# Optimization experiments

Hardware: AMD Instinct MI355X
Metric: run time of the kernel (lower is better)

## Reference

```python
import jax, jax.numpy as jnp
import numpy as np

TARGET_SIZE = (240, 320)
SCALE = 8
POS_MARGIN = 1.0
NEG_MARGIN = 0.2
POS_LAMBDA = 0.05
EPS = 1e-12


def _l2n(x, axis):
    # F.normalize(p=2): x / max(||x||, eps)
    n = jnp.sqrt(jnp.sum(x * x, axis=axis, keepdims=True))
    return x / jnp.maximum(n, EPS)


def _rodrigues(rv):
    # axis-angle [N,3] -> rotation matrix [N,3,3]
    theta = jnp.linalg.norm(rv, axis=-1, keepdims=True)
    k = rv / jnp.maximum(theta, EPS)
    kx, ky, kz = k[..., 0], k[..., 1], k[..., 2]
    z = jnp.zeros_like(kx)
    Km = jnp.stack([z, -kz, ky, kz, z, -kx, -ky, kx, z], axis=-1).reshape(rv.shape[:-1] + (3, 3))
    th = theta[..., None]
    I = jnp.eye(3, dtype=rv.dtype)
    return I + jnp.sin(th) * Km + (1.0 - jnp.cos(th)) * (Km @ Km)


def _plane_homography(rv0, t0, rv1, t1, n, d, K, Kinv):
    # plane-induced homography: H = K (R_0->1 - t_0->1 n^T / d) K^{-1}
    R0 = _rodrigues(rv0)
    R1 = _rodrigues(rv1)
    R = R1 @ jnp.swapaxes(R0, -1, -2)
    t = t1[..., None] - R @ t0[..., None]            # [N,3,1]
    return K @ (R - (t @ n) / d[..., None]) @ Kinv   # n:[N,1,3], d:[N,1]


def _scale_homography(H, origin, target):
    # sizes are (H, W); homography acts on (x, y, 1): H' = S H S^{-1}
    s = target / origin                               # [N,2] = (sy, sx)
    svec = jnp.stack([s[:, 1], s[:, 0], jnp.ones_like(s[:, 0])], axis=-1)  # (sx, sy, 1)
    return H * (svec[:, :, None] / svec[:, None, :])


def _coord_cells(Hc, Wc):
    xx, yy = jnp.meshgrid(jnp.arange(Wc), jnp.arange(Hc), indexing='xy')
    return jnp.stack([xx, yy], axis=-1).astype(jnp.float32) * SCALE  # [Hc,Wc,2] (x,y)


def _forward(pred_features, rotation_vector, translation_vectors, camera_nts,
             camera_depths, camera_Ks, camera_Kinvs, origin_sizes, interval_list):
    T, B, C = rotation_vector.shape[:3]
    TC = T * C
    Cf, Hc, Wc = pred_features.shape[-3:]
    M = Hc * Wc

    # permute [T,B,C,...] -> [T,C,B,...] -> flatten to [T*C,B,...] (matches torch permute+reshape)
    rv = jnp.transpose(rotation_vector, (0, 2, 1, 3)).reshape(TC, B, 3)
    tv = jnp.transpose(translation_vectors, (0, 2, 1, 3)).reshape(TC, B, 3)
    nts = jnp.transpose(camera_nts, (0, 2, 1, 3, 4)).reshape(TC, B, 1, 3)
    dep = jnp.transpose(camera_depths, (0, 2, 1, 3)).reshape(TC, B, 1)
    Ks = jnp.transpose(camera_Ks, (0, 2, 1, 3, 4)).reshape(TC, B, 3, 3)
    Kin = jnp.transpose(camera_Kinvs, (0, 2, 1, 3, 4)).reshape(TC, B, 3, 3)
    osz = jnp.transpose(origin_sizes, (0, 2, 1, 3)).reshape(TC, B, 2)

    coords = _coord_cells(Hc, Wc)                     # [Hc,Wc,2]
    target = jnp.asarray(TARGET_SIZE, jnp.float32)
    thresh = SCALE - 0.5

    def step(acc, xs):
        f0, f1, Htt = xs                              # f0,f1: [B,Cf,Hc,Wc], Htt: [B,3,3]
        d0 = _l2n(f0, 1)
        d1 = _l2n(f1, 1)
        dot = jax.nn.relu(jnp.einsum('bchw,bcHW->bhwHW', d0, d1))  # [B,Hc,Wc,Hc,Wc]
        dot = _l2n(dot.reshape(B, Hc, Wc, M), 3).reshape(B, Hc, Wc, Hc, Wc)
        dot = _l2n(dot.reshape(B, M, Hc, Wc), 1).reshape(B, Hc, Wc, Hc, Wc)
        pos = jax.nn.relu(POS_MARGIN - dot)
        neg = jax.nn.relu(dot - NEG_MARGIN)
        # warp frame-0 cell centers into frame 1
        pts = jnp.concatenate([jnp.broadcast_to(coords, (B, Hc, Wc, 2)),
                               jnp.ones((B, Hc, Wc, 1), f0.dtype)], axis=-1)
        w = jnp.einsum('bij,bhwj->bhwi', Htt, pts)
        z = w[..., 2:3]
        z = jnp.where(jnp.abs(z) < 1e-8, 1e-8, z)
        warped = w[..., :2] / z                       # [B,Hc,Wc,2]
        dist = jnp.linalg.norm(coords[None, None, None] - warped[:, :, :, None, None, :], axis=-1)
        mask = (dist <= thresh).astype(dot.dtype)     # [B,Hc,Wc,Hc,Wc]
        l = POS_LAMBDA * mask * pos + (1.0 - mask) * neg
        return acc + jnp.mean(l), None

    total = jnp.float32(0.0)
    for interval in interval_list:
        iv = int(interval)
        N = TC - iv
        flat = lambda a: a[:N].reshape((N * B,) + a.shape[2:])
        H_all = _plane_homography(flat(rv), flat(tv),
                                  rv[iv:].reshape(N * B, 3), tv[iv:].reshape(N * B, 3),
                                  flat(nts), flat(dep), flat(Ks), flat(Kin))
        H_all = _scale_homography(H_all, flat(osz), jnp.broadcast_to(target, (N * B, 2)))
        loss_i, _ = jax.lax.scan(step, jnp.float32(0.0),
                                 (pred_features[:N], pred_features[iv:], H_all.reshape(N, B, 3, 3)))
        total = total + loss_i / N
    return total / len(interval_list)


def setup_inputs() -> dict:
    key = jax.random.key(0)
    ks = jax.random.split(key, 8)
    T, B, C, Cf = 5, 2, 4, 32
    Hc, Wc = TARGET_SIZE[0] // SCALE, TARGET_SIZE[1] // SCALE
    pred = jax.random.normal(ks[0], (T * C, B, Cf, Hc, Wc), jnp.float32)
    rv = 0.1 * jax.random.normal(ks[1], (T, B, C, 3), jnp.float32)
    tv = 0.1 * jax.random.normal(ks[2], (T, B, C, 3), jnp.float32)
    nts = jnp.array([0.0, 0.0, -1.0], jnp.float32) + 0.05 * jax.random.normal(ks[3], (T, B, C, 1, 3), jnp.float32)
    dep = 1.0 + jax.random.uniform(ks[4], (T, B, C, 1), jnp.float32)
    fx = 300.0 + 200.0 * jax.random.uniform(ks[5], (T, B, C), jnp.float32)
    fy = fx * (0.95 + 0.1 * jax.random.uniform(ks[6], (T, B, C), jnp.float32))
    K = jnp.zeros((T, B, C, 3, 3), jnp.float32)
    K = K.at[..., 0, 0].set(fx).at[..., 1, 1].set(fy)
    K = K.at[..., 0, 2].set(320.0).at[..., 1, 2].set(240.0).at[..., 2, 2].set(1.0)
    Kinv = jnp.linalg.inv(K)
    osz = jnp.tile(jnp.array([480.0, 640.0], jnp.float32), (T, B, C, 1))
    return {
        'pred_features': pred,
        'rotation_vector': rv,
        'translation_vectors': tv,
        'camera_nts': nts,
        'camera_depths': dep,
        'camera_Ks': K,
        'camera_Kinvs': Kinv,
        'origin_sizes': osz,
        'interval_list': (1, 4),
    }


def reference(pred_features, rotation_vector, translation_vectors, camera_nts,
              camera_depths, camera_Ks, camera_Kinvs, origin_sizes, interval_list):
    return _forward(pred_features, rotation_vector, translation_vectors, camera_nts,
                    camera_depths, camera_Ks, camera_Kinvs, origin_sizes, interval_list)
```

## Files before the change

kernel.cpp:

```cpp
#include <hip/hip_runtime.h>
#include <math.h>

#define TT   5
#define CAM  4
#define TC   20
#define BB   2
#define CF   32
#define HC   30
#define WC   40
#define MM   1200
#define NMAX 19
#define EPSF 1e-12f
#define JT   75
#define RG4  19
#define RGB4 5
#define JSP  5
#define JQ   15
#define CT   5
#define REDB 16

typedef __attribute__((ext_vector_type(8))) short short8v;
typedef __attribute__((ext_vector_type(4))) float float4v;

__device__ inline unsigned short f2bf(float x) {
  unsigned int u = __float_as_uint(x);
  unsigned int r = (u + 0x7FFFu + ((u >> 16) & 1u)) >> 16;
  return (unsigned short)r;
}
__device__ inline float bf2f(unsigned short h) {
  return __uint_as_float(((unsigned int)h) << 16);
}

__device__ inline void rodrigues_d(const double rv[3], double R[9]) {
  double th = sqrt(rv[0]*rv[0] + rv[1]*rv[1] + rv[2]*rv[2]);
  double thc = fmax(th, 1e-12);
  double kx = rv[0] / thc, ky = rv[1] / thc, kz = rv[2] / thc;
  double st = sin(th), ct = cos(th);
  double Km[9] = { 0.0, -kz,  ky,  kz, 0.0, -kx,  -ky, kx, 0.0 };
  double K2[9];
  for (int r = 0; r < 3; ++r)
    for (int c = 0; c < 3; ++c)
      K2[r*3+c] = Km[r*3+0]*Km[0*3+c] + Km[r*3+1]*Km[1*3+c] + Km[r*3+2]*Km[2*3+c];
  for (int r = 0; r < 3; ++r)
    for (int c = 0; c < 3; ++c)
      R[r*3+c] = (r == c ? 1.0 : 0.0) + st * Km[r*3+c] + (1.0 - ct) * K2[r*3+c];
}
__device__ inline void mm3(const double* A, const double* B, double* C) {
  for (int r = 0; r < 3; ++r)
    for (int c = 0; c < 3; ++c)
      C[r*3+c] = A[r*3+0]*B[0*3+c] + A[r*3+1]*B[1*3+c] + A[r*3+2]*B[2*3+c];
}

__device__ inline bool decode_slot(int slot, const int* ivl, int& n, int& b, int& iv) {
  int ivi = slot / (NMAX * BB);
  int rem = slot % (NMAX * BB);
  n = rem / BB; b = rem % BB;
  iv = ivl[ivi];
  return n < TC - iv;
}

__global__ void k_prep(const float* __restrict__ pred, short8v* __restrict__ dsp,
                       const float* __restrict__ rv_, const float* __restrict__ tv_,
                       const float* __restrict__ nts_, const float* __restrict__ dep_,
                       const float* __restrict__ Ks_, const float* __restrict__ Kin_,
                       const float* __restrict__ osz_, const int* __restrict__ ivl,
                       float2* __restrict__ warped) {
  int bx = blockIdx.x;
  int tid = threadIdx.x;
  if (bx < TC * BB * 5) {
    int tb = bx / 5;
    int pix = (bx % 5) * 240 + tid;
    if (tid >= 240 || pix >= MM) return;
    const float* src = pred + (size_t)tb * CF * MM;
    short8v*     dst = dsp  + (size_t)tb * 4 * MM;
    float v[CF]; float ss = 0.f;
#pragma unroll
    for (int c = 0; c < CF; ++c) { float x = src[c * MM + pix]; v[c] = x; ss = fmaf(x, x, ss); }
    float inv = 1.f / fmaxf(sqrtf(ss), EPSF);
#pragma unroll
    for (int s = 0; s < 4; ++s) {
      short8v oh;
#pragma unroll
      for (int e = 0; e < 8; ++e) oh[e] = (short)f2bf(v[s*8+e] * inv);
      dst[(size_t)s * MM + pix] = oh;
    }
    return;
  }
  int slot = bx - TC * BB * 5;
  int n, b, iv;
  if (!decode_slot(slot, ivl, n, b, iv)) return;
  int q0 = n, q1 = n + iv;
  int t0 = q0 / CAM, c0 = q0 % CAM;
  int t1 = q1 / CAM, c1 = q1 % CAM;
  size_t e0 = (size_t)(t0 * BB + b) * CAM + c0;
  size_t e1 = (size_t)(t1 * BB + b) * CAM + c1;

  double rv0[3], tv0[3], rv1[3], tv1[3], nv[3];
  for (int k = 0; k < 3; ++k) {
    rv0[k] = rv_[e0*3 + k]; tv0[k] = tv_[e0*3 + k];
    rv1[k] = rv_[e1*3 + k]; tv1[k] = tv_[e1*3 + k];
    nv[k]  = nts_[e0*3 + k];
  }
  double d = dep_[e0];
  double K9[9], Ki9[9];
  for (int k = 0; k < 9; ++k) { K9[k] = Ks_[e0*9 + k]; Ki9[k] = Kin_[e0*9 + k]; }

  double R0[9], R1[9], R[9];
  rodrigues_d(rv0, R0);
  rodrigues_d(rv1, R1);
  for (int r = 0; r < 3; ++r)
    for (int c = 0; c < 3; ++c)
      R[r*3+c] = R1[r*3+0]*R0[c*3+0] + R1[r*3+1]*R0[c*3+1] + R1[r*3+2]*R0[c*3+2];
  double tvec[3];
  for (int r = 0; r < 3; ++r)
    tvec[r] = tv1[r] - (R[r*3+0]*tv0[0] + R[r*3+1]*tv0[1] + R[r*3+2]*tv0[2]);
  double Mid[9];
  for (int r = 0; r < 3; ++r)
    for (int c = 0; c < 3; ++c)
      Mid[r*3+c] = R[r*3+c] - tvec[r] * nv[c] / d;
  double T1[9], Hm[9];
  mm3(K9, Mid, T1);
  mm3(T1, Ki9, Hm);

  double osz0 = osz_[e0*2 + 0], osz1 = osz_[e0*2 + 1];
  double s0 = 240.0 / osz0, s1 = 320.0 / osz1;
  double sv[3] = { s1, s0, 1.0 };
  double Hs[9];
  for (int r = 0; r < 3; ++r)
    for (int c = 0; c < 3; ++c)
      Hs[r*3+c] = Hm[r*3+c] * sv[r] / sv[c];

  float2* wout = warped + (size_t)slot * MM;
  for (int cell = tid; cell < MM; cell += blockDim.x) {
    double x = (double)((cell % WC) * 8);
    double y = (double)((cell / WC) * 8);
    double wx = Hs[0]*x + Hs[1]*y + Hs[2];
    double wy = Hs[3]*x + Hs[4]*y + Hs[5];
    double wz = Hs[6]*x + Hs[7]*y + Hs[8];
    float z = (float)wz;
    if (fabsf(z) < 1e-8f) z = 1e-8f;
    wout[cell] = make_float2((float)wx / z, (float)wy / z);
  }
}

__device__ inline float4v s_tile1(short8v ah, short8v bh) {
  float4v acc = {0.f, 0.f, 0.f, 0.f};
  return __builtin_amdgcn_mfma_f32_16x16x32_bf16(ah, bh, acc, 0, 0, 0);
}

__global__ void __launch_bounds__(256) k_rnorm_p(const short8v* __restrict__ dsp,
                                                 const int* __restrict__ ivl,
                                                 float* __restrict__ prn) {
  int slot = blockIdx.x, jh = blockIdx.z;
  int n, b, iv;
  if (!decode_slot(slot, ivl, n, b, iv)) return;
  int wid = threadIdx.x >> 6, lane = threadIdx.x & 63;
  int rg = blockIdx.y * 4 + wid;
  if (rg >= RG4) return;
  int q = lane >> 4, li = lane & 15;
  int base = rg * 64;
  const short8v* D0 = dsp + (size_t)(n * BB + b) * 4 * MM;
  const short8v* B0 = dsp + (size_t)((n + iv) * BB + b) * 4 * MM + (size_t)q * MM + li;
  bool vt[4]; int rt[4];
  short8v ah[4];
  float4v racc[4];
#pragma unroll
  for (int t = 0; t < 4; ++t) {
    int rb = base + t * 16;
    vt[t] = rb < MM;
    rt[t] = vt[t] ? rb : 0;
    ah[t] = D0[(size_t)q * MM + rt[t] + li];
    racc[t] = (float4v){0.f, 0.f, 0.f, 0.f};
  }
  int jt0 = jh * JQ, jtN = jt0 + JQ;
  short8v bA = B0[jt0 * 16];
  short8v bB = B0[min(jt0 + 1, JT - 1) * 16];
#pragma unroll 3
  for (int jt = jt0; jt < jtN; ++jt) {
    short8v bC = B0[min(jt + 2, JT - 1) * 16];
#pragma unroll
    for (int t = 0; t < 4; ++t) {
      float4v acc = s_tile1(ah[t], bA);
#pragma unroll
      for (int r = 0; r < 4; ++r) {
        float x = fmaxf(acc[r], 0.f);
        racc[t][r] = fmaf(x, x, racc[t][r]);
      }
    }
    bA = bB; bB = bC;
  }
#pragma unroll
  for (int m = 1; m <= 8; m <<= 1)
#pragma unroll
    for (int t = 0; t < 4; ++t)
#pragma unroll
      for (int r = 0; r < 4; ++r)
        racc[t][r] += __shfl_xor(racc[t][r], m);
  if (li == 0) {
    float* o = prn + ((size_t)slot * JSP + jh) * MM;
#pragma unroll
    for (int t = 0; t < 4; ++t)
      if (vt[t]) {
#pragma unroll
        for (int r = 0; r < 4; ++r) o[rt[t] + q * 4 + r] = racc[t][r];
      }
  }
}

__global__ void __launch_bounds__(256) k_rnorm_fin(const float* __restrict__ prn,
                                                   const int* __restrict__ ivl,
                                                   float* __restrict__ irn) {
  int slot = blockIdx.x;
  int n, b, iv;
  if (!decode_slot(slot, ivl, n, b, iv)) return;
  int row = blockIdx.y * 256 + threadIdx.x;
  if (row >= MM) return;
  const float* p = prn + (size_t)slot * JSP * MM;
  float s = 0.f;
#pragma unroll
  for (int k = 0; k < JSP; ++k) s += p[k * MM + row];
  irn[(size_t)slot * MM + row] = 1.f / fmaxf(sqrtf(s), EPSF);
}

__global__ void __launch_bounds__(256) k_cnorm_p(const short8v* __restrict__ dsp,
                                                 const int* __restrict__ ivl,
                                                 const float* __restrict__ irn,
                                                 float* __restrict__ pcn) {
  int slot = blockIdx.x, jh = blockIdx.z;
  int n, b, iv;
  if (!decode_slot(slot, ivl, n, b, iv)) return;
  int wid = threadIdx.x >> 6, lane = threadIdx.x & 63;
  int rg = blockIdx.y * 4 + wid;
  if (rg >= RG4) return;
  int q = lane >> 4, li = lane & 15;
  int base = rg * 64;
  const short8v* D1 = dsp + (size_t)((n + iv) * BB + b) * 4 * MM;
  const short8v* B0 = dsp + (size_t)(n * BB + b) * 4 * MM + (size_t)q * MM + li;
  bool vt[4]; int rt[4];
  short8v ah[4];
  float4v cacc[4];
#pragma unroll
  for (int t = 0; t < 4; ++t) {
    int rb = base + t * 16;
    vt[t] = rb < MM;
    rt[t] = vt[t] ? rb : 0;
    ah[t] = D1[(size_t)q * MM + rt[t] + li];
    cacc[t] = (float4v){0.f, 0.f, 0.f, 0.f};
  }
  const float* irnS = irn + (size_t)slot * MM + li;
  int jt0 = jh * JQ, jtN = jt0 + JQ;
  short8v bA = B0[jt0 * 16];
  short8v bB = B0[min(jt0 + 1, JT - 1) * 16];
  float irA = irnS[jt0 * 16];
  float irB = irnS[min(jt0 + 1, JT - 1) * 16];
#pragma unroll 3
  for (int jt = jt0; jt < jtN; ++jt) {
    short8v bC = B0[min(jt + 2, JT - 1) * 16];
    float irC = irnS[min(jt + 2, JT - 1) * 16];
#pragma unroll
    for (int t = 0; t < 4; ++t) {
      float4v acc = s_tile1(ah[t], bA);
#pragma unroll
      for (int r = 0; r < 4; ++r) {
        float x = fmaxf(acc[r], 0.f) * irA;
        cacc[t][r] = fmaf(x, x, cacc[t][r]);
      }
    }
    bA = bB; bB = bC; irA = irB; irB = irC;
  }
#pragma unroll
  for (int m = 1; m <= 8; m <<= 1)
#pragma unroll
    for (int t = 0; t < 4; ++t)
#pragma unroll
      for (int r = 0; r < 4; ++r)
        cacc[t][r] += __shfl_xor(cacc[t][r], m);
  if (li == 0) {
    float* o = pcn + ((size_t)slot * JSP + jh) * MM;
#pragma unroll
    for (int t = 0; t < 4; ++t)
      if (vt[t]) {
#pragma unroll
        for (int r = 0; r < 4; ++r) o[rt[t] + q * 4 + r] = cacc[t][r];
      }
  }
}

__global__ void __launch_bounds__(256) k_cnorm_fin(const float* __restrict__ pcn,
                                                   const int* __restrict__ ivl,
                                                   float* __restrict__ icn) {
  int slot = blockIdx.x;
  int n, b, iv;
  if (!decode_slot(slot, ivl, n, b, iv)) return;
  int col = blockIdx.y * 256 + threadIdx.x;
  if (col >= MM) return;
  const float* p = pcn + (size_t)slot * JSP * MM;
  float s = 0.f;
#pragma unroll
  for (int k = 0; k < JSP; ++k) s += p[k * MM + col];
  icn[(size_t)slot * MM + col] = 1.f / fmaxf(sqrtf(s), EPSF);
}

__global__ void __launch_bounds__(256) k_loss(const short8v* __restrict__ dsp,
                                              const int* __restrict__ ivl,
                                              const float* __restrict__ irn,
                                              const float* __restrict__ icn,
                                              int niv,
                                              double* __restrict__ partials) {
  int slot = blockIdx.x, jh = blockIdx.z;
  int wid = threadIdx.x >> 6, lane = threadIdx.x & 63;
  int rg = blockIdx.y * 4 + wid;
  if (rg >= RG4) return;
  size_t pidx = ((size_t)slot * RG4 + rg) * JSP + jh;
  int n, b, iv;
  if (!decode_slot(slot, ivl, n, b, iv)) {
    if (lane == 0) partials[pidx] = 0.0;
    return;
  }
  int q = lane >> 4, li = lane & 15;
  int base = rg * 64;
  const short8v* D0 = dsp + (size_t)(n * BB + b) * 4 * MM;
  const short8v* B0 = dsp + (size_t)((n + iv) * BB + b) * 4 * MM + (size_t)q * MM + li;
  short8v ah[4];
  float u[4][4];
#pragma unroll
  for (int t = 0; t < 4; ++t) {
    int rb = base + t * 16;
    bool vt = rb < MM;
    int rtc = vt ? rb : 0;
    ah[t] = D0[(size_t)q * MM + rtc + li];
#pragma unroll
    for (int r = 0; r < 4; ++r)
      u[t][r] = vt ? irn[(size_t)slot * MM + rtc + q * 4 + r] : 0.f;
  }
  const float* icnS = icn + (size_t)slot * MM + li;
  int jt0 = jh * JQ, jtN = jt0 + JQ;
  short8v bA = B0[jt0 * 16];
  short8v bB = B0[min(jt0 + 1, JT - 1) * 16];
  float icA = icnS[jt0 * 16];
  float icB = icnS[min(jt0 + 1, JT - 1) * 16];
  float lacc0 = 0.f, lacc1 = 0.f;
#pragma unroll 3
  for (int jt = jt0; jt < jtN; ++jt) {
    short8v bC = B0[min(jt + 2, JT - 1) * 16];
    float icC = icnS[min(jt + 2, JT - 1) * 16];
#pragma unroll
    for (int t = 0; t < 4; ++t) {
      float4v acc = s_tile1(ah[t], bA);
      float s0 = fmaxf(fmaf(acc[0], icA * u[t][0], -0.2f), 0.f)
               + fmaxf(fmaf(acc[1], icA * u[t][1], -0.2f), 0.f);
      float s1 = fmaxf(fmaf(acc[2], icA * u[t][2], -0.2f), 0.f)
               + fmaxf(fmaf(acc[3], icA * u[t][3], -0.2f), 0.f);
      lacc0 += s0; lacc1 += s1;
    }
    bA = bB; bB = bC; icA = icB; icB = icC;
  }
  float lacc = lacc0 + lacc1;
#pragma unroll
  for (int off = 32; off > 0; off >>= 1) lacc += __shfl_xor(lacc, off);
  if (lane == 0) {
    double scale = 1.0 / ((double)(TC - iv) * BB * (double)MM * (double)MM * (double)niv);
    partials[pidx] = (double)lacc * scale;
  }
}

__global__ void __launch_bounds__(256) k_corr(const short8v* __restrict__ dsp,
                                              const int* __restrict__ ivl,
                                              const float* __restrict__ irn,
                                              const float* __restrict__ icn,
                                              const float2* __restrict__ warped,
                                              int niv,
                                              double* __restrict__ partials2) {
  __shared__ double swsum[4];
  int slot = blockIdx.x, tile = blockIdx.y;
  int t = threadIdx.x;
  int n, b, iv;
  bool valid = decode_slot(slot, ivl, n, b, iv);
  double corr = 0.0;
  int row = tile * 256 + t;
  if (valid && row < MM) {
    float2 wp = warped[(size_t)slot * MM + row];
    int kx0 = max(0, (int)ceilf((wp.x - 7.5f) * 0.125f));
    int kx1 = min(WC - 1, (int)floorf((wp.x + 7.5f) * 0.125f));
    int ky0 = max(0, (int)ceilf((wp.y - 7.5f) * 0.125f));
    int ky1 = min(HC - 1, (int)floorf((wp.y + 7.5f) * 0.125f));
    if (kx0 <= kx1 && ky0 <= ky1) {
      const short8v* D0 = dsp + (size_t)(n * BB + b) * 4 * MM;
      const short8v* D1 = dsp + (size_t)((n + iv) * BB + b) * 4 * MM;
      float a[CF];
#pragma unroll
      for (int qq = 0; qq < 4; ++qq) {
        short8v h = D0[(size_t)qq * MM + row];
#pragma unroll
        for (int e = 0; e < 8; ++e) a[qq * 8 + e] = bf2f((unsigned short)h[e]);
      }
      float ir = irn[(size_t)slot * MM + row];
      float fcorr = 0.f;
      for (int ky = ky0; ky <= ky1; ++ky) {
        for (int kx = kx0; kx <= kx1; ++kx) {
          float dx = (float)(kx * 8) - wp.x;
          float dy = (float)(ky * 8) - wp.y;
          if (fmaf(dx, dx, dy * dy) <= 56.25f) {
            int j = ky * WC + kx;
            float dot = 0.f;
#pragma unroll
            for (int qq = 0; qq < 4; ++qq) {
              short8v h1 = D1[(size_t)qq * MM + j];
#pragma unroll
              for (int e = 0; e < 8; ++e)
                dot = fmaf(a[qq * 8 + e], bf2f((unsigned short)h1[e]), dot);
            }
            float s = fmaxf(dot, 0.f);
            float D = s * ir * icn[(size_t)slot * MM + j];
            fcorr += 0.05f * fmaxf(1.f - D, 0.f) - fmaxf(D - 0.2f, 0.f);
          }
        }
      }
      double scale = 1.0 / ((double)(TC - iv) * BB * (double)MM * (double)MM * (double)niv);
      corr = (double)fcorr * scale;
    }
  }
#pragma unroll
  for (int off = 32; off > 0; off >>= 1) corr += __shfl_down(corr, off);
  int wid = t >> 6, lane = t & 63;
  if (lane == 0) swsum[wid] = corr;
  __syncthreads();
  if (t == 0) partials2[(size_t)slot * CT + tile] = swsum[0] + swsum[1] + swsum[2] + swsum[3];
}

__global__ void __launch_bounds__(256) k_red1(const double* __restrict__ p1, int n1,
                                              const double* __restrict__ p2, int n2,
                                              double* __restrict__ red) {
  __shared__ double sw[4];
  int t = threadIdx.x, blk = blockIdx.x;
  double s = 0.0;
  for (int i = blk * 256 + t; i < n1; i += REDB * 256) s += p1[i];
  for (int i = blk * 256 + t; i < n2; i += REDB * 256) s += p2[i];
#pragma unroll
  for (int off = 32; off > 0; off >>= 1) s += __shfl_down(s, off);
  int wid = t >> 6, lane = t & 63;
  if (lane == 0) sw[wid] = s;
  __syncthreads();
  if (t == 0) red[blk] = sw[0] + sw[1] + sw[2] + sw[3];
}

__global__ void k_red2(const double* __restrict__ red, float* __restrict__ out) {
  int lane = threadIdx.x;
  double s = (lane < REDB) ? red[lane] : 0.0;
#pragma unroll
  for (int off = 32; off > 0; off >>= 1) s += __shfl_down(s, off);
  if (lane == 0) out[0] = (float)s;
}

extern "C" void kernel_launch(void* const* d_in, const int* in_sizes, int n_in,
                              void* d_out, int out_size, void* d_ws, size_t ws_size,
                              hipStream_t stream) {
  const float* pred = (const float*)d_in[0];
  const float* rv   = (const float*)d_in[1];
  const float* tv   = (const float*)d_in[2];
  const float* nts  = (const float*)d_in[3];
  const float* dep  = (const float*)d_in[4];
  const float* Ks   = (const float*)d_in[5];
  const float* Kin  = (const float*)d_in[6];
  const float* osz  = (const float*)d_in[7];
  const int*   ivl  = (const int*)d_in[8];
  int niv = in_sizes[8];
  int slots = niv * NMAX * BB;

  char* ws = (char*)d_ws;
  size_t off = 0;
  short8v* dsp = (short8v*)(ws + off);  off += (size_t)TC * BB * 4 * MM * 16;
  float2* warped = (float2*)(ws + off); off += (size_t)slots * MM * 8;
  float* prn = (float*)(ws + off);      off += (size_t)slots * JSP * MM * 4;
  float* pcn = (float*)(ws + off);      off += (size_t)slots * JSP * MM * 4;
  float* irn = (float*)(ws + off);      off += (size_t)slots * MM * 4;
  float* icn = (float*)(ws + off);      off += (size_t)slots * MM * 4;
  off = (off + 255) & ~(size_t)255;
  double* partials = (double*)(ws + off);  off += (size_t)slots * RG4 * JSP * 8;
  double* partials2 = (double*)(ws + off); off += (size_t)slots * CT * 8;
  double* red = (double*)(ws + off);       off += (size_t)REDB * 8;

  int n1 = slots * RG4 * JSP;
  int n2 = slots * CT;

  hipLaunchKernelGGL(k_prep, dim3(TC * BB * 5 + slots), dim3(256), 0, stream,
                     pred, dsp, rv, tv, nts, dep, Ks, Kin, osz, ivl, warped);
  dim3 sgrid(slots, RGB4, JSP);
  dim3 fgrid(slots, CT);
  hipLaunchKernelGGL(k_rnorm_p, sgrid, dim3(256), 0, stream, dsp, ivl, prn);
  hipLaunchKernelGGL(k_rnorm_fin, fgrid, dim3(256), 0, stream, prn, ivl, irn);
  hipLaunchKernelGGL(k_cnorm_p, sgrid, dim3(256), 0, stream, dsp, ivl, irn, pcn);
  hipLaunchKernelGGL(k_cnorm_fin, fgrid, dim3(256), 0, stream, pcn, ivl, icn);
  hipLaunchKernelGGL(k_loss, sgrid, dim3(256), 0, stream, dsp, ivl, irn, icn, niv, partials);
  hipLaunchKernelGGL(k_corr, fgrid, dim3(256), 0, stream,
                     dsp, ivl, irn, icn, warped, niv, partials2);
  hipLaunchKernelGGL(k_red1, dim3(REDB), dim3(256), 0, stream, partials, n1, partials2, n2, red);
  hipLaunchKernelGGL(k_red2, dim3(1), dim3(64), 0, stream, red, (float*)d_out);
}
```

Measured before the change: 76.90 us.

## Fuse norm finalisation into consumers and merge loss, correlation and reductions

The separate row and column inverse-norm finalise kernels are removed. Each consumer now sums the split partial norms itself, into shared memory or registers, using rsqrt. The loss and correlation kernels are merged into a single launch that uses an extra grid z-slice, and the row scale is pre-multiplied into the bf16 A fragments. The two-stage final reduction becomes one block. Together these cut the launch count from nine to five, at the cost of redundant partial-sum reads and an extra bf16 rounding of the scaled features, which may change numerics slightly.

Measured after the change: 75.52 us. No clear change (-1.8%).

```diff
diff --git a/kernel.cpp b/kernel.cpp
--- a/kernel.cpp
+++ b/kernel.cpp
@@ -11,13 +11,13 @@
 #define MM   1200
 #define NMAX 19
 #define EPSF 1e-12f
+#define EPS2 1e-24f
 #define JT   75
 #define RG4  19
 #define RGB4 5
 #define JSP  5
 #define JQ   15
 #define CT   5
-#define REDB 16
 
 typedef __attribute__((ext_vector_type(8))) short short8v;
 typedef __attribute__((ext_vector_type(4))) float float4v;
@@ -174,10 +174,10 @@
   }
   int jt0 = jh * JQ, jtN = jt0 + JQ;
   short8v bA = B0[jt0 * 16];
-  short8v bB = B0[min(jt0 + 1, JT - 1) * 16];
+  short8v bB = B0[min(jt0 + 1, jtN - 1) * 16];
 #pragma unroll 3
   for (int jt = jt0; jt < jtN; ++jt) {
-    short8v bC = B0[min(jt + 2, JT - 1) * 16];
+    short8v bC = B0[min(jt + 2, jtN - 1) * 16];
 #pragma unroll
     for (int t = 0; t < 4; ++t) {
       float4v acc = s_tile1(ah[t], bA);
@@ -207,29 +207,26 @@
   }
 }
 
-__global__ void __launch_bounds__(256) k_rnorm_fin(const float* __restrict__ prn,
-                                                   const int* __restrict__ ivl,
-                                                   float* __restrict__ irn) {
-  int slot = blockIdx.x;
-  int n, b, iv;
-  if (!decode_slot(slot, ivl, n, b, iv)) return;
-  int row = blockIdx.y * 256 + threadIdx.x;
-  if (row >= MM) return;
-  const float* p = prn + (size_t)slot * JSP * MM;
-  float s = 0.f;
-#pragma unroll
-  for (int k = 0; k < JSP; ++k) s += p[k * MM + row];
-  irn[(size_t)slot * MM + row] = 1.f / fmaxf(sqrtf(s), EPSF);
-}
-
 __global__ void __launch_bounds__(256) k_cnorm_p(const short8v* __restrict__ dsp,
                                                  const int* __restrict__ ivl,
-                                                 const float* __restrict__ irn,
+                                                 const float* __restrict__ prn,
                                                  float* __restrict__ pcn) {
+  __shared__ float sIR[240];
   int slot = blockIdx.x, jh = blockIdx.z;
   int n, b, iv;
   if (!decode_slot(slot, ivl, n, b, iv)) return;
-  int wid = threadIdx.x >> 6, lane = threadIdx.x & 63;
+  int t = threadIdx.x;
+  int jt0 = jh * JQ, jtN = jt0 + JQ;
+  const float* prnS = prn + (size_t)slot * JSP * MM;
+  if (t < 240) {
+    int i = jt0 * 16 + t;
+    float s = 0.f;
+#pragma unroll
+    for (int k = 0; k < JSP; ++k) s += prnS[k * MM + i];
+    sIR[t] = rsqrtf(fmaxf(s, EPS2));
+  }
+  __syncthreads();
+  int wid = t >> 6, lane = t & 63;
   int rg = blockIdx.y * 4 + wid;
   if (rg >= RG4) return;
   int q = lane >> 4, li = lane & 15;
@@ -240,30 +237,29 @@
   short8v ah[4];
   float4v cacc[4];
 #pragma unroll
-  for (int t = 0; t < 4; ++t) {
-    int rb = base + t * 16;
-    vt[t] = rb < MM;
-    rt[t] = vt[t] ? rb : 0;
-    ah[t] = D1[(size_t)q * MM + rt[t] + li];
-    cacc[t] = (float4v){0.f, 0.f, 0.f, 0.f};
-  }
-  const float* irnS = irn + (size_t)slot * MM + li;
-  int jt0 = jh * JQ, jtN = jt0 + JQ;
+  for (int tt = 0; tt < 4; ++tt) {
+    int rb = base + tt * 16;
+    vt[tt] = rb < MM;
+    rt[tt] = vt[tt] ? rb : 0;
+    ah[tt] = D1[(size_t)q * MM + rt[tt] + li];
+    cacc[tt] = (float4v){0.f, 0.f, 0.f, 0.f};
+  }
   short8v bA = B0[jt0 * 16];
-  short8v bB = B0[min(jt0 + 1, JT - 1) * 16];
-  float irA = irnS[jt0 * 16];
-  float irB = irnS[min(jt0 + 1, JT - 1) * 16];
+  short8v bB = B0[min(jt0 + 1, jtN - 1) * 16];
+  float irA = sIR[li];
+  float irB = sIR[(min(jt0 + 1, jtN - 1) - jt0) * 16 + li];
 #pragma unroll 3
   for (int jt = jt0; jt < jtN; ++jt) {
-    short8v bC = B0[min(jt + 2, JT - 1) * 16];
-    float irC = irnS[min(jt + 2, JT - 1) * 16];
-#pragma unroll
-    for (int t = 0; t < 4; ++t) {
-      float4v acc = s_tile1(ah[t], bA);
+    int jn = min(jt + 2, jtN - 1);
+    short8v bC = B0[jn * 16];
+    float irC = sIR[(jn - jt0) * 16 + li];
+#pragma unroll
+    for (int tt = 0; tt < 4; ++tt) {
+      float4v acc = s_tile1(ah[tt], bA);
 #pragma unroll
       for (int r = 0; r < 4; ++r) {
         float x = fmaxf(acc[r], 0.f) * irA;
-        cacc[t][r] = fmaf(x, x, cacc[t][r]);
+        cacc[tt][r] = fmaf(x, x, cacc[tt][r]);
       }
     }
     bA = bB; bB = bC; irA = irB; irB = irC;
@@ -271,87 +267,161 @@
 #pragma unroll
   for (int m = 1; m <= 8; m <<= 1)
 #pragma unroll
-    for (int t = 0; t < 4; ++t)
+    for (int tt = 0; tt < 4; ++tt)
 #pragma unroll
       for (int r = 0; r < 4; ++r)
-        cacc[t][r] += __shfl_xor(cacc[t][r], m);
+        cacc[tt][r] += __shfl_xor(cacc[tt][r], m);
   if (li == 0) {
     float* o = pcn + ((size_t)slot * JSP + jh) * MM;
 #pragma unroll
-    for (int t = 0; t < 4; ++t)
-      if (vt[t]) {
-#pragma unroll
-        for (int r = 0; r < 4; ++r) o[rt[t] + q * 4 + r] = cacc[t][r];
+    for (int tt = 0; tt < 4; ++tt)
+      if (vt[tt]) {
+#pragma unroll
+        for (int r = 0; r < 4; ++r) o[rt[tt] + q * 4 + r] = cacc[tt][r];
       }
   }
 }
 
-__global__ void __launch_bounds__(256) k_cnorm_fin(const float* __restrict__ pcn,
-                                                   const int* __restrict__ ivl,
-                                                   float* __restrict__ icn) {
-  int slot = blockIdx.x;
+__global__ void __launch_bounds__(256) k_lc(const short8v* __restrict__ dsp,
+                                            const int* __restrict__ ivl,
+                                            const float* __restrict__ prn,
+                                            const float* __restrict__ pcn,
+                                            const float2* __restrict__ warped,
+                                            int niv,
+                                            double* __restrict__ partials,
+                                            double* __restrict__ partials2) {
+  __shared__ float sIC[240];
+  __shared__ float sLIR[256];
+  __shared__ double swsum[4];
+  int slot = blockIdx.x, y = blockIdx.y, z = blockIdx.z;
+  int t = threadIdx.x;
   int n, b, iv;
-  if (!decode_slot(slot, ivl, n, b, iv)) return;
-  int col = blockIdx.y * 256 + threadIdx.x;
-  if (col >= MM) return;
-  const float* p = pcn + (size_t)slot * JSP * MM;
-  float s = 0.f;
-#pragma unroll
-  for (int k = 0; k < JSP; ++k) s += p[k * MM + col];
-  icn[(size_t)slot * MM + col] = 1.f / fmaxf(sqrtf(s), EPSF);
-}
-
-__global__ void __launch_bounds__(256) k_loss(const short8v* __restrict__ dsp,
-                                              const int* __restrict__ ivl,
-                                              const float* __restrict__ irn,
-                                              const float* __restrict__ icn,
-                                              int niv,
-                                              double* __restrict__ partials) {
-  int slot = blockIdx.x, jh = blockIdx.z;
-  int wid = threadIdx.x >> 6, lane = threadIdx.x & 63;
-  int rg = blockIdx.y * 4 + wid;
+  bool valid = decode_slot(slot, ivl, n, b, iv);
+  const float* prnS = prn + (size_t)slot * JSP * MM;
+  const float* pcnS = pcn + (size_t)slot * JSP * MM;
+
+  if (z == JSP) {
+    double corr = 0.0;
+    int row = y * 256 + t;
+    if (valid && row < MM) {
+      float2 wp = warped[(size_t)slot * MM + row];
+      int kx0 = max(0, (int)ceilf((wp.x - 7.5f) * 0.125f));
+      int kx1 = min(WC - 1, (int)floorf((wp.x + 7.5f) * 0.125f));
+      int ky0 = max(0, (int)ceilf((wp.y - 7.5f) * 0.125f));
+      int ky1 = min(HC - 1, (int)floorf((wp.y + 7.5f) * 0.125f));
+      if (kx0 <= kx1 && ky0 <= ky1) {
+        const short8v* D0 = dsp + (size_t)(n * BB + b) * 4 * MM;
+        const short8v* D1 = dsp + (size_t)((n + iv) * BB + b) * 4 * MM;
+        float a[CF];
+#pragma unroll
+        for (int qq = 0; qq < 4; ++qq) {
+          short8v h = D0[(size_t)qq * MM + row];
+#pragma unroll
+          for (int e = 0; e < 8; ++e) a[qq * 8 + e] = bf2f((unsigned short)h[e]);
+        }
+        float irs = 0.f;
+#pragma unroll
+        for (int k = 0; k < JSP; ++k) irs += prnS[k * MM + row];
+        float ir = rsqrtf(fmaxf(irs, EPS2));
+        float fcorr = 0.f;
+        for (int ky = ky0; ky <= ky1; ++ky) {
+          for (int kx = kx0; kx <= kx1; ++kx) {
+            float dx = (float)(kx * 8) - wp.x;
+            float dy = (float)(ky * 8) - wp.y;
+            if (fmaf(dx, dx, dy * dy) <= 56.25f) {
+              int j = ky * WC + kx;
+              float dot = 0.f;
+#pragma unroll
+              for (int qq = 0; qq < 4; ++qq) {
+                short8v h1 = D1[(size_t)qq * MM + j];
+#pragma unroll
+                for (int e = 0; e < 8; ++e)
+                  dot = fmaf(a[qq * 8 + e], bf2f((unsigned short)h1[e]), dot);
+              }
+              float ics = 0.f;
+#pragma unroll
+              for (int k = 0; k < JSP; ++k) ics += pcnS[k * MM + j];
+              float ic = rsqrtf(fmaxf(ics, EPS2));
+              float s = fmaxf(dot, 0.f);
+              float D = s * ir * ic;
+              fcorr += 0.05f * fmaxf(1.f - D, 0.f) - fmaxf(D - 0.2f, 0.f);
+            }
+          }
+        }
+        double scale = 1.0 / ((double)(TC - iv) * BB * (double)MM * (double)MM * (double)niv);
+        corr = (double)fcorr * scale;
+      }
+    }
+#pragma unroll
+    for (int off = 32; off > 0; off >>= 1) corr += __shfl_down(corr, off);
+    int wid = t >> 6, lane = t & 63;
+    if (lane == 0) swsum[wid] = corr;
+    __syncthreads();
+    if (t == 0) partials2[(size_t)slot * CT + y] = swsum[0] + swsum[1] + swsum[2] + swsum[3];
+    return;
+  }
+
+  int wid = t >> 6, lane = t & 63;
+  int rg = y * 4 + wid;
+  if (!valid) {
+    if (lane == 0 && rg < RG4) partials[((size_t)slot * RG4 + rg) * JSP + z] = 0.0;
+    return;
+  }
+  int jt0 = z * JQ, jtN = jt0 + JQ;
+  if (t < 240) {
+    int j = jt0 * 16 + t;
+    float s = 0.f;
+#pragma unroll
+    for (int k = 0; k < JSP; ++k) s += pcnS[k * MM + j];
+    sIC[t] = rsqrtf(fmaxf(s, EPS2));
+  }
+  {
+    int row = y * 256 + t;
+    float v = 0.f;
+    if (row < MM) {
+      float s = 0.f;
+#pragma unroll
+      for (int k = 0; k < JSP; ++k) s += prnS[k * MM + row];
+      v = rsqrtf(fmaxf(s, EPS2));
+    }
+    sLIR[t] = v;
+  }
+  __syncthreads();
   if (rg >= RG4) return;
-  size_t pidx = ((size_t)slot * RG4 + rg) * JSP + jh;
-  int n, b, iv;
-  if (!decode_slot(slot, ivl, n, b, iv)) {
-    if (lane == 0) partials[pidx] = 0.0;
-    return;
-  }
   int q = lane >> 4, li = lane & 15;
   int base = rg * 64;
   const short8v* D0 = dsp + (size_t)(n * BB + b) * 4 * MM;
   const short8v* B0 = dsp + (size_t)((n + iv) * BB + b) * 4 * MM + (size_t)q * MM + li;
   short8v ah[4];
-  float u[4][4];
-#pragma unroll
-  for (int t = 0; t < 4; ++t) {
-    int rb = base + t * 16;
+#pragma unroll
+  for (int t4 = 0; t4 < 4; ++t4) {
+    int rb = base + t4 * 16;
     bool vt = rb < MM;
     int rtc = vt ? rb : 0;
-    ah[t] = D0[(size_t)q * MM + rtc + li];
-#pragma unroll
-    for (int r = 0; r < 4; ++r)
-      u[t][r] = vt ? irn[(size_t)slot * MM + rtc + q * 4 + r] : 0.f;
-  }
-  const float* icnS = icn + (size_t)slot * MM + li;
-  int jt0 = jh * JQ, jtN = jt0 + JQ;
+    short8v a = D0[(size_t)q * MM + rtc + li];
+    float sc = vt ? sLIR[wid * 64 + t4 * 16 + li] : 0.f;
+#pragma unroll
+    for (int e = 0; e < 8; ++e)
+      a[e] = (short)f2bf(bf2f((unsigned short)a[e]) * sc);
+    ah[t4] = a;
+  }
   short8v bA = B0[jt0 * 16];
-  short8v bB = B0[min(jt0 + 1, JT - 1) * 16];
-  float icA = icnS[jt0 * 16];
-  float icB = icnS[min(jt0 + 1, JT - 1) * 16];
+  short8v bB = B0[min(jt0 + 1, jtN - 1) * 16];
+  float icA = sIC[li];
+  float icB = sIC[(min(jt0 + 1, jtN - 1) - jt0) * 16 + li];
   float lacc0 = 0.f, lacc1 = 0.f;
 #pragma unroll 3
   for (int jt = jt0; jt < jtN; ++jt) {
-    short8v bC = B0[min(jt + 2, JT - 1) * 16];
-    float icC = icnS[min(jt + 2, JT - 1) * 16];
-#pragma unroll
-    for (int t = 0; t < 4; ++t) {
-      float4v acc = s_tile1(ah[t], bA);
-      float s0 = fmaxf(fmaf(acc[0], icA * u[t][0], -0.2f), 0.f)
-               + fmaxf(fmaf(acc[1], icA * u[t][1], -0.2f), 0.f);
-      float s1 = fmaxf(fmaf(acc[2], icA * u[t][2], -0.2f), 0.f)
-               + fmaxf(fmaf(acc[3], icA * u[t][3], -0.2f), 0.f);
-      lacc0 += s0; lacc1 += s1;
+    int jn = min(jt + 2, jtN - 1);
+    short8v bC = B0[jn * 16];
+    float icC = sIC[(jn - jt0) * 16 + li];
+#pragma unroll
+    for (int t4 = 0; t4 < 4; ++t4) {
+      float4v acc = s_tile1(ah[t4], bA);
+      lacc0 += fmaxf(fmaf(acc[0], icA, -0.2f), 0.f)
+             + fmaxf(fmaf(acc[1], icA, -0.2f), 0.f);
+      lacc1 += fmaxf(fmaf(acc[2], icA, -0.2f), 0.f)
+             + fmaxf(fmaf(acc[3], icA, -0.2f), 0.f);
     }
     bA = bB; bB = bC; icA = icB; icB = icC;
   }
@@ -360,96 +430,24 @@
   for (int off = 32; off > 0; off >>= 1) lacc += __shfl_xor(lacc, off);
   if (lane == 0) {
     double scale = 1.0 / ((double)(TC - iv) * BB * (double)MM * (double)MM * (double)niv);
-    partials[pidx] = (double)lacc * scale;
-  }
-}
-
-__global__ void __launch_bounds__(256) k_corr(const short8v* __restrict__ dsp,
-                                              const int* __restrict__ ivl,
-                                              const float* __restrict__ irn,
-                                              const float* __restrict__ icn,
-                                              const float2* __restrict__ warped,
-                                              int niv,
-                                              double* __restrict__ partials2) {
-  __shared__ double swsum[4];
-  int slot = blockIdx.x, tile = blockIdx.y;
+    partials[((size_t)slot * RG4 + rg) * JSP + z] = (double)lacc * scale;
+  }
+}
+
+__global__ void __launch_bounds__(256) k_red(const double* __restrict__ p1, int n1,
+                                             const double* __restrict__ p2, int n2,
+                                             float* __restrict__ out) {
+  __shared__ double sw[4];
   int t = threadIdx.x;
-  int n, b, iv;
-  bool valid = decode_slot(slot, ivl, n, b, iv);
-  double corr = 0.0;
-  int row = tile * 256 + t;
-  if (valid && row < MM) {
-    float2 wp = warped[(size_t)slot * MM + row];
-    int kx0 = max(0, (int)ceilf((wp.x - 7.5f) * 0.125f));
-    int kx1 = min(WC - 1, (int)floorf((wp.x + 7.5f) * 0.125f));
-    int ky0 = max(0, (int)ceilf((wp.y - 7.5f) * 0.125f));
-    int ky1 = min(HC - 1, (int)floorf((wp.y + 7.5f) * 0.125f));
-    if (kx0 <= kx1 && ky0 <= ky1) {
-      const short8v* D0 = dsp + (size_t)(n * BB + b) * 4 * MM;
-      const short8v* D1 = dsp + (size_t)((n + iv) * BB + b) * 4 * MM;
-      float a[CF];
-#pragma unroll
-      for (int qq = 0; qq < 4; ++qq) {
-        short8v h = D0[(size_t)qq * MM + row];
-#pragma unroll
-        for (int e = 0; e < 8; ++e) a[qq * 8 + e] = bf2f((unsigned short)h[e]);
-      }
-      float ir = irn[(size_t)slot * MM + row];
-      float fcorr = 0.f;
-      for (int ky = ky0; ky <= ky1; ++ky) {
-        for (int kx = kx0; kx <= kx1; ++kx) {
-          float dx = (float)(kx * 8) - wp.x;
-          float dy = (float)(ky * 8) - wp.y;
-          if (fmaf(dx, dx, dy * dy) <= 56.25f) {
-            int j = ky * WC + kx;
-            float dot = 0.f;
-#pragma unroll
-            for (int qq = 0; qq < 4; ++qq) {
-              short8v h1 = D1[(size_t)qq * MM + j];
-#pragma unroll
-              for (int e = 0; e < 8; ++e)
-                dot = fmaf(a[qq * 8 + e], bf2f((unsigned short)h1[e]), dot);
-            }
-            float s = fmaxf(dot, 0.f);
-            float D = s * ir * icn[(size_t)slot * MM + j];
-            fcorr += 0.05f * fmaxf(1.f - D, 0.f) - fmaxf(D - 0.2f, 0.f);
-          }
-        }
-      }
-      double scale = 1.0 / ((double)(TC - iv) * BB * (double)MM * (double)MM * (double)niv);
-      corr = (double)fcorr * scale;
-    }
-  }
-#pragma unroll
-  for (int off = 32; off > 0; off >>= 1) corr += __shfl_down(corr, off);
-  int wid = t >> 6, lane = t & 63;
-  if (lane == 0) swsum[wid] = corr;
-  __syncthreads();
-  if (t == 0) partials2[(size_t)slot * CT + tile] = swsum[0] + swsum[1] + swsum[2] + swsum[3];
-}
-
-__global__ void __launch_bounds__(256) k_red1(const double* __restrict__ p1, int n1,
-                                              const double* __restrict__ p2, int n2,
-                                              double* __restrict__ red) {
-  __shared__ double sw[4];
-  int t = threadIdx.x, blk = blockIdx.x;
   double s = 0.0;
-  for (int i = blk * 256 + t; i < n1; i += REDB * 256) s += p1[i];
-  for (int i = blk * 256 + t; i < n2; i += REDB * 256) s += p2[i];
+  for (int i = t; i < n1; i += 256) s += p1[i];
+  for (int i = t; i < n2; i += 256) s += p2[i];
 #pragma unroll
   for (int off = 32; off > 0; off >>= 1) s += __shfl_down(s, off);
   int wid = t >> 6, lane = t & 63;
   if (lane == 0) sw[wid] = s;
   __syncthreads();
-  if (t == 0) red[blk] = sw[0] + sw[1] + sw[2] + sw[3];
-}
-
-__global__ void k_red2(const double* __restrict__ red, float* __restrict__ out) {
-  int lane = threadIdx.x;
-  double s = (lane < REDB) ? red[lane] : 0.0;
-#pragma unroll
-  for (int off = 32; off > 0; off >>= 1) s += __shfl_down(s, off);
-  if (lane == 0) out[0] = (float)s;
+  if (t == 0) out[0] = (float)(sw[0] + sw[1] + sw[2] + sw[3]);
 }
 
 extern "C" void kernel_launch(void* const* d_in, const int* in_sizes, int n_in,
@@ -473,12 +471,9 @@
   float2* warped = (float2*)(ws + off); off += (size_t)slots * MM * 8;
   float* prn = (float*)(ws + off);      off += (size_t)slots * JSP * MM * 4;
   float* pcn = (float*)(ws + off);      off += (size_t)slots * JSP * MM * 4;
-  float* irn = (float*)(ws + off);      off += (size_t)slots * MM * 4;
-  float* icn = (float*)(ws + off);      off += (size_t)slots * MM * 4;
   off = (off + 255) & ~(size_t)255;
   double* partials = (double*)(ws + off);  off += (size_t)slots * RG4 * JSP * 8;
   double* partials2 = (double*)(ws + off); off += (size_t)slots * CT * 8;
-  double* red = (double*)(ws + off);       off += (size_t)REDB * 8;
 
   int n1 = slots * RG4 * JSP;
   int n2 = slots * CT;
@@ -486,14 +481,10 @@
   hipLaunchKernelGGL(k_prep, dim3(TC * BB * 5 + slots), dim3(256), 0, stream,
                      pred, dsp, rv, tv, nts, dep, Ks, Kin, osz, ivl, warped);
   dim3 sgrid(slots, RGB4, JSP);
-  dim3 fgrid(slots, CT);
   hipLaunchKernelGGL(k_rnorm_p, sgrid, dim3(256), 0, stream, dsp, ivl, prn);
-  hipLaunchKernelGGL(k_rnorm_fin, fgrid, dim3(256), 0, stream, prn, ivl, irn);
-  hipLaunchKernelGGL(k_cnorm_p, sgrid, dim3(256), 0, stream, dsp, ivl, irn, pcn);
-  hipLaunchKernelGGL(k_cnorm_fin, fgrid, dim3(256), 0, stream, pcn, ivl, icn);
-  hipLaunchKernelGGL(k_loss, sgrid, dim3(256), 0, stream, dsp, ivl, irn, icn, niv, partials);
-  hipLaunchKernelGGL(k_corr, fgrid, dim3(256), 0, stream,
-                     dsp, ivl, irn, icn, warped, niv, partials2);
-  hipLaunchKernelGGL(k_red1, dim3(REDB), dim3(256), 0, stream, partials, n1, partials2, n2, red);
-  hipLaunchKernelGGL(k_red2, dim3(1), dim3(64), 0, stream, red, (float*)d_out);
-}
+  hipLaunchKernelGGL(k_cnorm_p, sgrid, dim3(256), 0, stream, dsp, ivl, prn, pcn);
+  hipLaunchKernelGGL(k_lc, dim3(slots, RGB4, JSP + 1), dim3(256), 0, stream,
+                     dsp, ivl, prn, pcn, warped, niv, partials, partials2);
+  hipLaunchKernelGGL(k_red, dim3(1), dim3(256), 0, stream, partials, n1, partials2, n2,
+                     (float*)d_out);
+}
```
